# Kernel tuning notes

Hardware: AMD Instinct MI355X
Metric: run time of the kernel (lower is better)

## Reference

```python
import jax, jax.numpy as jnp
import numpy as np

ALPHA = 0.2  # LeakyReLU negative slope
NEG_INF = -9e15  # matches torch's -9000000000000000.0 mask value


def setup_inputs() -> dict:
    key = jax.random.key(0)
    k1, k2, k3, k4 = jax.random.split(key, 4)
    B, M, F = 8, 1024, 256
    H, E = 8, F // 8  # attention_heads, out_features
    x = jax.random.normal(k1, (B, M, F), dtype=jnp.float32)
    adj = jax.random.randint(k2, (B, M, M), 0, 2, dtype=jnp.int32)
    weight = jax.random.normal(k3, (H, F, E), dtype=jnp.float32)
    att = jax.random.normal(k4, (H, 2 * E, 1), dtype=jnp.float32)
    return {"x": x, "adj": adj, "weight": weight, "att": att}


def reference(x, adj, weight, att):
    # x: [B, M, F], adj: [B, M, M], weight: [H, F, E], att: [H, 2E, 1]
    B, M, _ = x.shape
    H, _, E = weight.shape
    Wh = jnp.einsum('bmf,hfe->bhme', x, weight)  # [B, H, M, E]
    # Decompose the repeat+concat score: e_ij = a1.Wh_i + a2.Wh_j
    a1 = att[:, :E, 0]   # [H, E]
    a2 = att[:, E:, 0]   # [H, E]
    s1 = jnp.einsum('bhme,he->bhm', Wh, a1)
    s2 = jnp.einsum('bhme,he->bhm', Wh, a2)
    e = s1[:, :, :, None] + s2[:, :, None, :]  # [B, H, M, M]
    e = jnp.where(e > 0, e, ALPHA * e)  # LeakyReLU
    e = jnp.where(adj[:, None, :, :] > 0, e, NEG_INF)
    attn = jax.nn.softmax(e, axis=-1)  # [B, H, M, M]
    h = jnp.einsum('bhmn,bhne->bhme', attn, Wh)  # [B, H, M, E]
    out = h.transpose(0, 2, 1, 3).reshape(B, M, H * E)  # concat heads
    out = jax.nn.elu(out)  # res_pre_act path (dropout is identity in eval)
    return out
```

## Files before the change

### kernel.cpp

```cpp
#include <hip/hip_runtime.h>
#include <stdint.h>

#define ALPHA 0.2f
#define LOG2E 1.44269504089f

typedef __attribute__((ext_vector_type(8))) short s16x8;
typedef __attribute__((ext_vector_type(4))) float f32x4;
typedef __attribute__((ext_vector_type(4))) unsigned u32x4;

__device__ __forceinline__ unsigned short f2bf(float f) {
    union { float f; unsigned u; } c; c.f = f;
    unsigned u = c.u;
    u += 0x7fffu + ((u >> 16) & 1u);
    return (unsigned short)(u >> 16);
}

__global__ void k_prep_w(const float* __restrict__ weight, const float* __restrict__ att,
                         unsigned short* __restrict__ wT, float* __restrict__ wa1,
                         float* __restrict__ wa2) {
    int blk = blockIdx.x, t = threadIdx.x;
    if (blk < 256) {
        int c = blk, h = c >> 5, e = c & 31;
        wT[c * 256 + t] = f2bf(weight[h * 8192 + t * 32 + e]);
    } else {
        int id = blk - 256, h = id >> 1, which = id & 1;
        float s = 0.f;
        for (int e = 0; e < 32; ++e)
            s += weight[h * 8192 + t * 32 + e] * att[h * 64 + which * 32 + e];
        s *= LOG2E;
        (which ? wa2 : wa1)[h * 256 + t] = s;
    }
}

__global__ void __launch_bounds__(512) k_pre(const int* __restrict__ adj,
                                             unsigned* __restrict__ gmask,
                                             const float* __restrict__ x,
                                             const unsigned short* __restrict__ wT,
                                             const float* __restrict__ wa1,
                                             const float* __restrict__ wa2,
                                             float* __restrict__ s1,
                                             float* __restrict__ s2,
                                             unsigned short* __restrict__ WhT) {
    __shared__ unsigned char adjb[16][1024];
    __shared__ float xs[16][260];
    __shared__ unsigned short x16s[16][256];
    int blk = blockIdx.x;
    int t = threadIdx.x, w = t >> 6, l = t & 63;
    int b = blk >> 6;
    const int* abase = adj + blk * 16384;
#pragma unroll
    for (int it = 0; it < 8; ++it) {
        int f = it * 512 + t;
        int4 v = *(const int4*)(abase + f * 4);
        int row = f >> 8, col = (f & 255) * 4;
        unsigned p1 = __builtin_amdgcn_perm((unsigned)v.y, (unsigned)v.x, 0x00000400u);
        unsigned p2 = __builtin_amdgcn_perm((unsigned)v.w, (unsigned)v.z, 0x00000400u);
        unsigned pk = __builtin_amdgcn_perm(p2, p1, 0x05040100u);
        *(unsigned*)&adjb[row][col ^ ((row & 7) << 4)] = pk;
    }
    const float* xbase = x + blk * 4096;
#pragma unroll
    for (int it = 0; it < 2; ++it) {
        int f = it * 512 + t;
        float4 xv = *(const float4*)(xbase + f * 4);
        int row = f >> 6, col = (f & 63) * 4;
        *(float4*)&xs[row][col] = xv;
        ushort4 hv;
        hv.x = f2bf(xv.x); hv.y = f2bf(xv.y); hv.z = f2bf(xv.z); hv.w = f2bf(xv.w);
        *(ushort4*)((char*)&x16s[0][0] + ((row * 512 + col * 2) ^ ((row & 7) << 4))) = hv;
    }
    __syncthreads();
    if (w < 4) {
        for (int k = 0; k < 64; ++k) {
            int task = w * 64 + k;
            int row = task >> 4, ch = task & 15;
            unsigned char byv = adjb[row][(ch * 64 + l) ^ ((row & 7) << 4)];
            unsigned long long mk = __ballot(byv != 0);
            if (l == 0) {
                unsigned* dst = gmask + (blk * 16 + row) * 32 + ch * 2;
                dst[0] = (unsigned)mk;
                dst[1] = (unsigned)(mk >> 32);
            }
        }
    } else {
        int td = (w - 4) * 64 + l;
        int row = td & 15, grp = td >> 4;
        int h = grp >> 1, which = grp & 1;
        const float* wap = (which ? wa2 : wa1) + h * 256;
        float s = 0.f;
#pragma unroll 4
        for (int f = 0; f < 256; f += 4) {
            f32x4 xv = *(const f32x4*)&xs[row][f];
            f32x4 wv = *(const f32x4*)&wap[f];
            s += xv[0] * wv[0] + xv[1] * wv[1] + xv[2] * wv[2] + xv[3] * wv[3];
        }
        int m = (blk & 63) * 16 + row;
        (which ? s2 : s1)[(b * 8 + h) * 1024 + m] = s;
    }
    int lrow = l & 15, lk = l >> 4;
#pragma unroll
    for (int ct = 0; ct < 2; ++ct) {
        int c0 = (w * 2 + ct) * 16;
        f32x4 acc = {0, 0, 0, 0};
        const unsigned short* ap = wT + (c0 + lrow) * 256 + lk * 8;
#pragma unroll
        for (int k0 = 0; k0 < 256; k0 += 32) {
            s16x8 af = *(const s16x8*)(ap + k0);
            s16x8 bf = *(const s16x8*)((char*)&x16s[0][0] +
                        ((lrow * 512 + (lk * 8 + k0) * 2) ^ ((lrow & 7) << 4)));
            acc = __builtin_amdgcn_mfma_f32_16x16x32_bf16(af, bf, acc, 0, 0, 0);
        }
#pragma unroll
        for (int j = 0; j < 4; ++j) {
            int c = c0 + lk * 4 + j;
            WhT[(b * 256 + c) * 1024 + (blk & 63) * 16 + lrow] = f2bf(acc[j]);
        }
    }
}

__global__ void __launch_bounds__(512, 4) k_attn(const unsigned* __restrict__ gmask,
                                                 const float* __restrict__ s1,
                                                 const float* __restrict__ s2,
                                                 const unsigned short* __restrict__ WhT,
                                                 float* __restrict__ out) {
    __shared__ float s2s[4][1024];
    __shared__ unsigned amaskw[16][36];
    __shared__ float s1s[4][16];
    __shared__ float mxsh[4][16][2];
    __shared__ float accsh[4][64][13];
    int bid = blockIdx.x;
    int o = (bid & 7) * 128 + (bid >> 3);
    int b = o >> 7, r = o & 127;
    int mt = r >> 1, m0 = mt * 16, hg = (r & 1) * 4;
    int t = threadIdx.x, w = t >> 6, l = t & 63;
    int hd = w & 3, nh = w >> 2;
    for (int i = t; i < 4096; i += 512)
        s2s[i >> 10][i & 1023] = s2[b * 8192 + hg * 1024 + i];
    amaskw[t >> 5][t & 31] = gmask[(b * 1024 + m0) * 32 + t];
    if (t < 64) s1s[t >> 4][t & 15] = s1[b * 8192 + (hg + (t >> 4)) * 1024 + m0 + (t & 15)];
    __syncthreads();
    int m = l & 15, q = l >> 4;
    int h = hg + hd;
    int nbase = nh * 512;
    u32x4 mv0 = *(const u32x4*)&amaskw[m][nh * 16];
    u32x4 mv1 = *(const u32x4*)&amaskw[m][nh * 16 + 4];
    u32x4 mv2 = *(const u32x4*)&amaskw[m][nh * 16 + 8];
    u32x4 mv3 = *(const u32x4*)&amaskw[m][nh * 16 + 12];
    float mx01 = -3.0e38f, mx23 = -3.0e38f, mx45 = -3.0e38f, mx67 = -3.0e38f;
#pragma unroll
    for (int i = 0; i < 16; ++i) {
        unsigned word = (i < 4 ? mv0[i & 3] : i < 8 ? mv1[i & 3] : i < 12 ? mv2[i & 3]
                                                                          : mv3[i & 3]);
        unsigned wm8 = word >> (q * 8);
        int nn = nbase + i * 32 + q * 8;
        f32x4 svA = *(const f32x4*)&s2s[hd][nn];
        f32x4 svB = *(const f32x4*)&s2s[hd][nn + 4];
        float c0 = (wm8 & 1u)   ? svA[0] : -3.0e38f;
        float c1 = (wm8 & 2u)   ? svA[1] : -3.0e38f;
        float c2 = (wm8 & 4u)   ? svA[2] : -3.0e38f;
        float c3 = (wm8 & 8u)   ? svA[3] : -3.0e38f;
        float c4 = (wm8 & 16u)  ? svB[0] : -3.0e38f;
        float c5 = (wm8 & 32u)  ? svB[1] : -3.0e38f;
        float c6 = (wm8 & 64u)  ? svB[2] : -3.0e38f;
        float c7 = (wm8 & 128u) ? svB[3] : -3.0e38f;
        mx01 = fmaxf(mx01, fmaxf(c0, c1));
        mx23 = fmaxf(mx23, fmaxf(c2, c3));
        mx45 = fmaxf(mx45, fmaxf(c4, c5));
        mx67 = fmaxf(mx67, fmaxf(c6, c7));
    }
    float mxs2 = fmaxf(fmaxf(mx01, mx23), fmaxf(mx45, mx67));
    mxs2 = fmaxf(mxs2, __shfl_xor(mxs2, 16));
    mxs2 = fmaxf(mxs2, __shfl_xor(mxs2, 32));
    if (l < 16) mxsh[hd][l][nh] = mxs2;
    __syncthreads();
    float mxf = fmaxf(mxsh[hd][m][0], mxsh[hd][m][1]);
    float s1v = s1s[hd][m];
    float mxr = s1v + mxf;
    float mx = fmaxf(mxr, ALPHA * mxr);
    float cc1 = s1v - mx;
    float cc2 = fmaf(ALPHA, s1v, -mx);
    f32x4 acc0 = {0,0,0,0}, acc1 = {0,0,0,0}, accs = {0,0,0,0};
    s16x8 ones;
#pragma unroll
    for (int u = 0; u < 8; ++u) ones[u] = (short)0x3F80;
    const unsigned short* bp0 = WhT + (b * 8 + h) * 32768 + m * 1024 + q * 8 + nbase;
    const unsigned short* bp1 = bp0 + 16 * 1024;
#pragma unroll
    for (int i = 0; i < 16; ++i) {
        int n0 = i * 32;
        unsigned word = (i < 4 ? mv0[i & 3] : i < 8 ? mv1[i & 3] : i < 12 ? mv2[i & 3]
                                                                          : mv3[i & 3]);
        unsigned wm8 = word >> (q * 8);
        int nn = nbase + n0 + q * 8;
        f32x4 svA = *(const f32x4*)&s2s[hd][nn];
        f32x4 svB = *(const f32x4*)&s2s[hd][nn + 4];
        float pv[8];
#pragma unroll
        for (int u = 0; u < 8; ++u) {
            float sv = (u < 4 ? svA[u] : svB[u - 4]);
            float arg = fmaxf(sv + cc1, fmaf(ALPHA, sv, cc2));
            arg = ((wm8 >> u) & 1u) ? arg : -3.0e38f;
            pv[u] = __builtin_amdgcn_exp2f(arg);
        }
        u32x4 aw;
#pragma unroll
        for (int p = 0; p < 4; ++p) {
            union { float f; unsigned u; } lo, hi;
            lo.f = pv[2 * p]; hi.f = pv[2 * p + 1];
            aw[p] = __builtin_amdgcn_perm(hi.u, lo.u, 0x07060302u);
        }
        s16x8 af = __builtin_bit_cast(s16x8, aw);
        s16x8 bf0 = *(const s16x8*)(bp0 + n0);
        s16x8 bf1 = *(const s16x8*)(bp1 + n0);
        acc0 = __builtin_amdgcn_mfma_f32_16x16x32_bf16(af, bf0, acc0, 0, 0, 0);
        acc1 = __builtin_amdgcn_mfma_f32_16x16x32_bf16(af, bf1, acc1, 0, 0, 0);
        accs = __builtin_amdgcn_mfma_f32_16x16x32_bf16(af, ones, accs, 0, 0, 0);
    }
    if (nh == 1) {
#pragma unroll
        for (int j = 0; j < 4; ++j) {
            accsh[hd][l][j]     = acc0[j];
            accsh[hd][l][4 + j] = acc1[j];
            accsh[hd][l][8 + j] = accs[j];
        }
    }
    __syncthreads();
    if (nh == 0) {
#pragma unroll
        for (int j = 0; j < 4; ++j) {
            float a0 = acc0[j] + accsh[hd][l][j];
            float a1 = acc1[j] + accsh[hd][l][4 + j];
            float as = accs[j] + accsh[hd][l][8 + j];
            float inv = 1.f / as;
            float v0 = a0 * inv;
            float v1 = a1 * inv;
            v0 = v0 > 0.f ? v0 : __expf(v0) - 1.f;
            v1 = v1 > 0.f ? v1 : __expf(v1) - 1.f;
            int mrow = q * 4 + j;
            float* op = &out[(b * 1024 + m0 + mrow) * 256 + h * 32];
            op[m] = v0;
            op[16 + m] = v1;
        }
    }
}

extern "C" void kernel_launch(void* const* d_in, const int* in_sizes, int n_in,
                              void* d_out, int out_size, void* d_ws, size_t ws_size,
                              hipStream_t stream) {
    const float* x      = (const float*)d_in[0];
    const int*   adj    = (const int*)d_in[1];
    const float* weight = (const float*)d_in[2];
    const float* att    = (const float*)d_in[3];

    char* ws = (char*)d_ws;
    unsigned short* wT  = (unsigned short*)(ws);
    unsigned short* WhT = (unsigned short*)(ws + 131072);
    float* s1  = (float*)(ws + 4325376);
    float* s2  = (float*)(ws + 4587520);
    float* wa1 = (float*)(ws + 4849664);
    float* wa2 = (float*)(ws + 4857856);
    unsigned* gmask = (unsigned*)(ws + 4866048);
    float* out = (float*)d_out;

    k_prep_w<<<272, 256, 0, stream>>>(weight, att, wT, wa1, wa2);
    k_pre<<<512, 512, 0, stream>>>(adj, gmask, x, wT, wa1, wa2, s1, s2, WhT);
    k_attn<<<1024, 512, 0, stream>>>(gmask, s1, s2, WhT, out);
}
```

Before: 68.80 us.

## Precompute per-head top-16 s2 candidates to replace the masked row-max scan

Adds a small kernel that finds, for each batch and head, the 16 largest s2 values and their indices. The attention kernel then bounds each row's masked max by checking only those 16 candidates against the adjacency bitmask, falling back to the 16th-largest value. This replaces the full 1024-column masked max pass and one block barrier in the attention kernel. The result is an upper bound on the true masked max, and softmax is shift-invariant, so the output stays correct. The cost is an extra kernel launch with a serial top-k loop, plus a little extra workspace.

```diff
diff --git a/kernel.cpp b/kernel.cpp
--- a/kernel.cpp
+++ b/kernel.cpp
@@ -118,15 +118,49 @@
     }
 }
 
+__global__ void __launch_bounds__(64) k_top(const float* __restrict__ s2,
+                                            float* __restrict__ tval,
+                                            unsigned* __restrict__ tidx) {
+    int bh = blockIdx.x, l = threadIdx.x;
+    const float* p = s2 + bh * 1024;
+    float v[16];
+#pragma unroll
+    for (int k = 0; k < 4; ++k) {
+        f32x4 x4 = *(const f32x4*)(p + l * 16 + k * 4);
+        v[k * 4 + 0] = x4[0]; v[k * 4 + 1] = x4[1];
+        v[k * 4 + 2] = x4[2]; v[k * 4 + 3] = x4[3];
+    }
+    unsigned used = 0;
+    for (int r = 0; r < 16; ++r) {
+        float lmax = -3.0e38f; int larg = 0;
+#pragma unroll
+        for (int k = 0; k < 16; ++k) {
+            float c = ((used >> k) & 1u) ? -3.0e38f : v[k];
+            if (c > lmax) { lmax = c; larg = k; }
+        }
+        float wmax = lmax;
+#pragma unroll
+        for (int off = 32; off >= 1; off >>= 1) wmax = fmaxf(wmax, __shfl_xor(wmax, off));
+        unsigned long long hm = __ballot(lmax == wmax);
+        int fl = (int)__builtin_ctzll(hm);
+        if (l == fl) {
+            tval[bh * 16 + r] = wmax;
+            tidx[bh * 16 + r] = (unsigned)(l * 16 + larg);
+            used |= 1u << larg;
+        }
+    }
+}
+
 __global__ void __launch_bounds__(512, 4) k_attn(const unsigned* __restrict__ gmask,
                                                  const float* __restrict__ s1,
                                                  const float* __restrict__ s2,
+                                                 const float* __restrict__ tval,
+                                                 const unsigned* __restrict__ tidx,
                                                  const unsigned short* __restrict__ WhT,
                                                  float* __restrict__ out) {
     __shared__ float s2s[4][1024];
     __shared__ unsigned amaskw[16][36];
     __shared__ float s1s[4][16];
-    __shared__ float mxsh[4][16][2];
     __shared__ float accsh[4][64][13];
     int bid = blockIdx.x;
     int o = (bid & 7) * 128 + (bid >> 3);
@@ -142,43 +176,25 @@
     int m = l & 15, q = l >> 4;
     int h = hg + hd;
     int nbase = nh * 512;
+    const float*    tv = tval + (b * 8 + h) * 16;
+    const unsigned* ti = tidx + (b * 8 + h) * 16;
+    float mxs2 = tv[15];
+#pragma unroll
+    for (int j = 0; j < 16; ++j) {
+        unsigned id = ti[j];
+        unsigned wd = amaskw[m][id >> 5];
+        unsigned bit = (wd >> (id & 31u)) & 1u;
+        mxs2 = fmaxf(mxs2, bit ? tv[j] : -3.0e38f);
+    }
+    float s1v = s1s[hd][m];
+    float mxr = s1v + mxs2;
+    float mx = fmaxf(mxr, ALPHA * mxr);
+    float cc1 = s1v - mx;
+    float cc2 = fmaf(ALPHA, s1v, -mx);
     u32x4 mv0 = *(const u32x4*)&amaskw[m][nh * 16];
     u32x4 mv1 = *(const u32x4*)&amaskw[m][nh * 16 + 4];
     u32x4 mv2 = *(const u32x4*)&amaskw[m][nh * 16 + 8];
     u32x4 mv3 = *(const u32x4*)&amaskw[m][nh * 16 + 12];
-    float mx01 = -3.0e38f, mx23 = -3.0e38f, mx45 = -3.0e38f, mx67 = -3.0e38f;
-#pragma unroll
-    for (int i = 0; i < 16; ++i) {
-        unsigned word = (i < 4 ? mv0[i & 3] : i < 8 ? mv1[i & 3] : i < 12 ? mv2[i & 3]
-                                                                          : mv3[i & 3]);
-        unsigned wm8 = word >> (q * 8);
-        int nn = nbase + i * 32 + q * 8;
-        f32x4 svA = *(const f32x4*)&s2s[hd][nn];
-        f32x4 svB = *(const f32x4*)&s2s[hd][nn + 4];
-        float c0 = (wm8 & 1u)   ? svA[0] : -3.0e38f;
-        float c1 = (wm8 & 2u)   ? svA[1] : -3.0e38f;
-        float c2 = (wm8 & 4u)   ? svA[2] : -3.0e38f;
-        float c3 = (wm8 & 8u)   ? svA[3] : -3.0e38f;
-        float c4 = (wm8 & 16u)  ? svB[0] : -3.0e38f;
-        float c5 = (wm8 & 32u)  ? svB[1] : -3.0e38f;
-        float c6 = (wm8 & 64u)  ? svB[2] : -3.0e38f;
-        float c7 = (wm8 & 128u) ? svB[3] : -3.0e38f;
-        mx01 = fmaxf(mx01, fmaxf(c0, c1));
-        mx23 = fmaxf(mx23, fmaxf(c2, c3));
-        mx45 = fmaxf(mx45, fmaxf(c4, c5));
-        mx67 = fmaxf(mx67, fmaxf(c6, c7));
-    }
-    float mxs2 = fmaxf(fmaxf(mx01, mx23), fmaxf(mx45, mx67));
-    mxs2 = fmaxf(mxs2, __shfl_xor(mxs2, 16));
-    mxs2 = fmaxf(mxs2, __shfl_xor(mxs2, 32));
-    if (l < 16) mxsh[hd][l][nh] = mxs2;
-    __syncthreads();
-    float mxf = fmaxf(mxsh[hd][m][0], mxsh[hd][m][1]);
-    float s1v = s1s[hd][m];
-    float mxr = s1v + mxf;
-    float mx = fmaxf(mxr, ALPHA * mxr);
-    float cc1 = s1v - mx;
-    float cc2 = fmaf(ALPHA, s1v, -mx);
     f32x4 acc0 = {0,0,0,0}, acc1 = {0,0,0,0}, accs = {0,0,0,0};
     s16x8 ones;
 #pragma unroll
@@ -260,9 +276,12 @@
     float* wa1 = (float*)(ws + 4849664);
     float* wa2 = (float*)(ws + 4857856);
     unsigned* gmask = (unsigned*)(ws + 4866048);
+    float*    tval  = (float*)(ws + 5914624);
+    unsigned* tidx  = (unsigned*)(ws + 5918720);
     float* out = (float*)d_out;
 
     k_prep_w<<<272, 256, 0, stream>>>(weight, att, wT, wa1, wa2);
     k_pre<<<512, 512, 0, stream>>>(adj, gmask, x, wT, wa1, wa2, s1, s2, WhT);
-    k_attn<<<1024, 512, 0, stream>>>(gmask, s1, s2, WhT, out);
-}
+    k_top<<<64, 64, 0, stream>>>(s2, tval, tidx);
+    k_attn<<<1024, 512, 0, stream>>>(gmask, s1, s2, tval, tidx, WhT, out);
+}
```

Measured after the change: 76.37 us. +11.0%, slower.
